# Performance work log

Hardware: AMD Instinct MI355X
Metric: run time of the kernel (lower is better)

Reference implementation:

```python
import jax, jax.numpy as jnp
import numpy as np

H = 1024
E = 8
K = 2
N = 16384
LN_EPS = 1e-5


def _layernorm(h, g, b):
    m = jnp.mean(h, axis=-1, keepdims=True)
    v = jnp.mean(jnp.square(h - m), axis=-1, keepdims=True)
    return (h - m) * jax.lax.rsqrt(v + LN_EPS) * g + b


def setup_inputs() -> dict:
    key = jax.random.key(0)
    ks = jax.random.split(key, 8)
    s = 0.02
    return {
        "x": jax.random.normal(ks[0], (N, H), dtype=jnp.float32),
        "Wg": jax.random.normal(ks[1], (H, E), dtype=jnp.float32) * s,
        "bg": jnp.zeros((E,), dtype=jnp.float32),
        "W1": jax.random.normal(ks[2], (E, H, H), dtype=jnp.float32) * s,
        "b1": jnp.zeros((E, H), dtype=jnp.float32),
        "g1": jnp.ones((E, H), dtype=jnp.float32),
        "be1": jnp.zeros((E, H), dtype=jnp.float32),
        "W2": jax.random.normal(ks[3], (E, H, H), dtype=jnp.float32) * s,
        "b2": jnp.zeros((E, H), dtype=jnp.float32),
        "g2": jnp.ones((E, H), dtype=jnp.float32),
        "be2": jnp.zeros((E, H), dtype=jnp.float32),
    }


def reference(x, Wg, bg, W1, b1, g1, be1, W2, b2, g2, be2):
    # Gating: softmax over experts, top-k, renormalize
    gate_probs = jax.nn.softmax(x @ Wg + bg, axis=1)            # [N, E]
    tk_p, tk_i = jax.lax.top_k(gate_probs, K)                    # [N, K]
    tk_p = tk_p / (jnp.sum(tk_p, axis=1, keepdims=True) + 1e-9)
    # Dense per-expert combine weight (zero where expert not selected)
    w = jnp.sum(tk_p[:, :, None] * jax.nn.one_hot(tk_i, E, dtype=x.dtype), axis=1)  # [N, E]

    # ResidualBlock per expert, computed densely for all tokens (dropout = eval/no-op)
    h = jnp.einsum('nh,eho->eno', x, W1) + b1[:, None, :]        # [E, N, H]
    h = jax.nn.relu(_layernorm(h, g1[:, None, :], be1[:, None, :]))
    h = jnp.einsum('enh,eho->eno', h, W2) + b2[:, None, :]
    h = _layernorm(h, g2[:, None, :], be2[:, None, :])
    y = jax.nn.relu(x[None, :, :] + h)                           # [E, N, H]

    moe_out = jnp.einsum('ne,enh->nh', w, y)                     # [N, H]
    return moe_out, gate_probs
```

## Files before the change

kernel.cpp:

```cpp
#include <hip/hip_runtime.h>
#include <cstdint>
#include <cstddef>

constexpr int H_DIM = 1024;
constexpr int NE    = 8;
constexpr int NT    = 16384;
constexpr int NP    = NT * 2;

constexpr int BM = 128, BN = 128, BK = 32;
constexpr int NKT = H_DIM / BK;
constexpr int MAX_WG = (NP / BM + NE) * (H_DIM / BN);

typedef __attribute__((ext_vector_type(8)))  short          short8;
typedef __attribute__((ext_vector_type(8)))  unsigned short ushort8;
typedef __attribute__((ext_vector_type(4)))  float          f32x4;
typedef __attribute__((ext_vector_type(16))) float          f32x16;

__device__ __forceinline__ unsigned short f2bf(float f) {
  union { float f; uint32_t u; } c; c.f = f;
  uint32_t u = c.u;
  u = (u + 0x7fffu + ((u >> 16) & 1u)) >> 16;
  return (unsigned short)u;
}
__device__ __forceinline__ float bf2f(unsigned short h) {
  union { uint32_t u; float f; } c; c.u = ((uint32_t)h) << 16;
  return c.f;
}

__device__ __forceinline__ void gload16(const unsigned short* g, unsigned short* l) {
  __builtin_amdgcn_global_load_lds((const __attribute__((address_space(1))) void*)g,
                                   (__attribute__((address_space(3))) void*)l, 16, 0, 0);
}

__global__ __launch_bounds__(256) void prep_kernel(
    const float* __restrict__ X, const float* __restrict__ Wg,
    const float* __restrict__ bg, unsigned short* __restrict__ Xb,
    float* __restrict__ gate_out, int* __restrict__ tk_e, float* __restrict__ tk_w,
    const float* __restrict__ W1, const float* __restrict__ W2,
    unsigned short* __restrict__ T1, unsigned short* __restrict__ T2)
{
  __shared__ float tile[64][65];
  int b = blockIdx.x;
  if (b >= 4096) {
    int t = b - 4096;
    int zi = t >> 8;
    const float* W = (zi < 8) ? W1 : W2;
    unsigned short* T = (zi < 8) ? T1 : T2;
    int e  = zi & 7;
    int o0 = ((t >> 4) & 15) * 64;
    int h0 = (t & 15) * 64;
    int c  = threadIdx.x & 63;
    int r0 = (threadIdx.x >> 6) * 16;
    const float* src = W + ((size_t)e * H_DIM + h0) * H_DIM + o0;
#pragma unroll
    for (int i = 0; i < 16; ++i)
      tile[r0 + i][c] = src[(size_t)(r0 + i) * H_DIM + c];
    __syncthreads();
    unsigned short* dst = T + ((size_t)e * H_DIM + o0) * H_DIM + h0;
#pragma unroll
    for (int i = 0; i < 16; ++i)
      dst[(size_t)(r0 + i) * H_DIM + c] = f2bf(tile[c][r0 + i]);
    return;
  }

  int wid = threadIdx.x >> 6, lane = threadIdx.x & 63;
  int n = b * 4 + wid;
  const float* xr = X + (size_t)n * H_DIM;

  const float4* xp = (const float4*)(xr + lane * 16);
  float4 f0 = xp[0], f1 = xp[1], f2 = xp[2], f3 = xp[3];
  float v[16] = {f0.x,f0.y,f0.z,f0.w, f1.x,f1.y,f1.z,f1.w,
                 f2.x,f2.y,f2.z,f2.w, f3.x,f3.y,f3.z,f3.w};

  ushort8 u0, u1;
#pragma unroll
  for (int j = 0; j < 8; ++j) { u0[j] = f2bf(v[j]); u1[j] = f2bf(v[8 + j]); }
  ushort8* xb = (ushort8*)(Xb + (size_t)n * H_DIM + lane * 16);
  xb[0] = u0; xb[1] = u1;

  float acc[8];
#pragma unroll
  for (int e = 0; e < 8; ++e) acc[e] = 0.f;
#pragma unroll
  for (int j = 0; j < 16; ++j) {
    int h = lane * 16 + j;
    const float4* wg = (const float4*)(Wg + (size_t)h * 8);
    float4 a = wg[0], bb = wg[1];
    float xv = v[j];
    acc[0] += xv * a.x;  acc[1] += xv * a.y;  acc[2] += xv * a.z;  acc[3] += xv * a.w;
    acc[4] += xv * bb.x; acc[5] += xv * bb.y; acc[6] += xv * bb.z; acc[7] += xv * bb.w;
  }
#pragma unroll
  for (int m = 1; m < 64; m <<= 1) {
#pragma unroll
    for (int e = 0; e < 8; ++e) acc[e] += __shfl_xor(acc[e], m);
  }
#pragma unroll
  for (int e = 0; e < 8; ++e) acc[e] += bg[e];

  float mx = acc[0];
#pragma unroll
  for (int e = 1; e < 8; ++e) mx = fmaxf(mx, acc[e]);
  float g[8], s = 0.f;
#pragma unroll
  for (int e = 0; e < 8; ++e) { g[e] = __expf(acc[e] - mx); s += g[e]; }
  float inv = 1.f / s;
#pragma unroll
  for (int e = 0; e < 8; ++e) g[e] *= inv;

  int e0 = 0; float b0 = g[0];
#pragma unroll
  for (int e = 1; e < 8; ++e) if (g[e] > b0) { b0 = g[e]; e0 = e; }
  int e1 = -1; float b1v = -1.f;
#pragma unroll
  for (int e = 0; e < 8; ++e) if (e != e0 && g[e] > b1v) { b1v = g[e]; e1 = e; }
  float s2 = b0 + b1v + 1e-9f;

  if (lane == 0) {
    float4* gp = (float4*)(gate_out + (size_t)n * 8);
    gp[0] = make_float4(g[0], g[1], g[2], g[3]);
    gp[1] = make_float4(g[4], g[5], g[6], g[7]);
    tk_e[2 * n] = e0; tk_e[2 * n + 1] = e1;
    tk_w[2 * n] = b0 / s2; tk_w[2 * n + 1] = b1v / s2;
  }
}

__global__ __launch_bounds__(256) void hist_kernel(
    const int* __restrict__ tk_e, int* __restrict__ blockHist)
{
  __shared__ int h[8];
  if (threadIdx.x < 8) h[threadIdx.x] = 0;
  __syncthreads();
  int i0 = blockIdx.x * 512 + threadIdx.x;
  atomicAdd(&h[tk_e[i0]], 1);
  atomicAdd(&h[tk_e[i0 + 256]], 1);
  __syncthreads();
  if (threadIdx.x < 8) blockHist[blockIdx.x * 8 + threadIdx.x] = h[threadIdx.x];
}

__global__ void scan_worklist_kernel(const int* __restrict__ blockHist,
                                     int* __restrict__ blockBase,
                                     int* __restrict__ count, int* __restrict__ offs,
                                     int* __restrict__ wl, int* __restrict__ wlCount)
{
  __shared__ int nmt[8], ebase[8], totalS;
  int e = threadIdx.x;
  if (e < 8) {
    int run = 0;
    for (int b = 0; b < 64; ++b) { blockBase[b * 8 + e] = run; run += blockHist[b * 8 + e]; }
    count[e] = run;
  }
  __syncthreads();
  if (threadIdx.x == 0) {
    int o = 0, wo = 0;
    for (int k = 0; k < 8; ++k) {
      offs[k] = o; o += count[k];
      nmt[k] = (count[k] + BM - 1) / BM;
      ebase[k] = wo; wo += nmt[k] * (H_DIM / BN);
    }
    totalS = wo; wlCount[0] = wo;
  }
  __syncthreads();
  if (e < 8) {
    int o = offs[e];
    for (int b = 0; b < 64; ++b) blockBase[b * 8 + e] += o;
  }
  int total = totalS;
  for (int i = threadIdx.x; i < total; i += blockDim.x) {
    int ee = 0;
    while (ee < 7 && i >= ebase[ee + 1]) ++ee;
    int loc = i - ebase[ee];
    int nt = loc / nmt[ee];
    int mt = loc - nt * nmt[ee];
    wl[i] = (ee << 20) | (nt << 16) | mt;
  }
}

__global__ __launch_bounds__(256) void place_kernel(
    const int* __restrict__ tk_e, const int* __restrict__ blockBase,
    int* __restrict__ pairTok, int* __restrict__ pairExp, int* __restrict__ slots)
{
  __shared__ int cur[8];
  if (threadIdx.x < 8) cur[threadIdx.x] = blockBase[blockIdx.x * 8 + threadIdx.x];
  __syncthreads();
#pragma unroll
  for (int j = 0; j < 2; ++j) {
    int i = blockIdx.x * 512 + j * 256 + threadIdx.x;
    int e = tk_e[i];
    int s = atomicAdd(&cur[e], 1);
    pairTok[s] = i >> 1; pairExp[s] = e; slots[i] = s;
  }
}

template<bool GATHER>
__global__ __launch_bounds__(256, 3) void gemm32_kernel(
    const unsigned short* __restrict__ Ab,
    const unsigned short* __restrict__ Bt,
    const float* __restrict__ bias,
    const int* __restrict__ pairTok,
    const int* __restrict__ count, const int* __restrict__ offs,
    const int* __restrict__ wl, const int* __restrict__ wlCount,
    unsigned short* __restrict__ Out)
{
  __shared__ unsigned short As[3 * 4096];
  __shared__ unsigned short Bs[3 * 4096];

  const int total = wlCount[0];
  const int orig = blockIdx.x;
  if (orig >= total) return;
  const int qq = total >> 3, rr = total & 7;
  const int xcd = orig & 7, sub = orig >> 3;
  const int idx = (xcd < rr ? xcd * (qq + 1) : rr * (qq + 1) + (xcd - rr) * qq) + sub;
  const int ent = wl[idx];
  const int e = ent >> 20, ntb = (ent >> 16) & 15, mtb = ent & 0xffff;
  const int cnt = count[e], base = offs[e];

  const int tid = threadIdx.x;
  const int wid = tid >> 6, l = tid & 63;
  const int wr = wid >> 1, wc = wid & 1;

  const int rsub = (l >> 2);
  const int kswz = ((l & 3) * 8) ^ (((l >> 5) & 1) << 4);

  const unsigned short *apg0, *apg1, *bpg0, *bpg1;
  {
    int r0 = wid * 16 + rsub;
    int r1 = 64 + wid * 16 + rsub;
    int g0 = mtb * BM + r0; if (g0 >= cnt) g0 = cnt - 1;
    int g1 = mtb * BM + r1; if (g1 >= cnt) g1 = cnt - 1;
    size_t a0, a1;
    if (GATHER) { a0 = (size_t)pairTok[base + g0]; a1 = (size_t)pairTok[base + g1]; }
    else        { a0 = (size_t)(base + g0);        a1 = (size_t)(base + g1); }
    apg0 = Ab + a0 * H_DIM + kswz;
    apg1 = Ab + a1 * H_DIM + kswz;
    const unsigned short* bb = Bt + ((size_t)e * H_DIM + ntb * BN) * H_DIM + kswz;
    bpg0 = bb + (size_t)r0 * H_DIM;
    bpg1 = bb + (size_t)r1 * H_DIM;
  }

  const int lrow = (l & 15) * 64 + ((l >> 4) & 1) * 1024;
  const int sw = ((l >> 3) & 1) << 5;
  const int kb0 = (((l >> 5) * 16) + 0)  ^ sw;
  const int kb1 = (((l >> 5) * 16) + 32) ^ sw;

  auto STAGE = [&](int u, int sl) {
    unsigned short* ad = As + sl * 4096 + wid * 512;
    unsigned short* bd = Bs + sl * 4096 + wid * 512;
    gload16(apg0 + (size_t)u * BK, ad);
    gload16(apg1 + (size_t)u * BK, ad + 2048);
    gload16(bpg0 + (size_t)u * BK, bd);
    gload16(bpg1 + (size_t)u * BK, bd + 2048);
  };

  STAGE(0, 0); STAGE(1, 1);
  asm volatile("s_waitcnt vmcnt(4)" ::: "memory");
  __builtin_amdgcn_s_barrier();

  f32x16 acc[2][2] = {};

  int sl = 0, sstage = 2;
  for (int t = 0; t < NKT; ++t) {
    const char* aB = (const char*)As + sl * 8192 + wr * 4096 + lrow;
    const char* bB = (const char*)Bs + sl * 8192 + wc * 4096 + lrow;

    short8 af[2][2], bf[2][2];
#pragma unroll
    for (int j = 0; j < 2; ++j) {
      af[j][0] = *(const short8*)(aB + j * 2048 + kb0);
      af[j][1] = *(const short8*)(aB + j * 2048 + kb1);
      bf[j][0] = *(const short8*)(bB + j * 2048 + kb0);
      bf[j][1] = *(const short8*)(bB + j * 2048 + kb1);
    }

    if (t + 2 < NKT) STAGE(t + 2, sstage);

    __builtin_amdgcn_s_setprio(1);
#pragma unroll
    for (int ks = 0; ks < 2; ++ks)
#pragma unroll
      for (int j = 0; j < 2; ++j)
#pragma unroll
        for (int r = 0; r < 2; ++r)
          acc[j][r] = __builtin_amdgcn_mfma_f32_32x32x16_bf16(af[j][ks], bf[r][ks], acc[j][r], 0, 0, 0);
    __builtin_amdgcn_s_setprio(0);

    if (t + 2 < NKT)       asm volatile("s_waitcnt vmcnt(4)" ::: "memory");
    else if (t + 2 == NKT) asm volatile("s_waitcnt vmcnt(0)" ::: "memory");
    __builtin_amdgcn_s_barrier();

    sl = (sl == 2) ? 0 : sl + 1;
    sstage = (sstage == 2) ? 0 : sstage + 1;
  }

  float bvv[2];
#pragma unroll
  for (int r = 0; r < 2; ++r)
    bvv[r] = bias[e * H_DIM + ntb * BN + wc * 64 + r * 32 + (l & 31)];
#pragma unroll
  for (int j = 0; j < 2; ++j)
#pragma unroll
    for (int r = 0; r < 2; ++r) {
      int gcol = ntb * BN + wc * 64 + r * 32 + (l & 31);
#pragma unroll
      for (int reg = 0; reg < 16; ++reg) {
        int row = mtb * BM + wr * 64 + j * 32 + (reg & 3) + 8 * (reg >> 2) + 4 * (l >> 5);
        if (row < cnt)
          Out[(size_t)(base + row) * H_DIM + gcol] = f2bf(acc[j][r][reg] + bvv[r]);
      }
    }
}

__global__ __launch_bounds__(256) void ln_relu_kernel(
    unsigned short* __restrict__ buf, const float* __restrict__ gamma,
    const float* __restrict__ beta, const int* __restrict__ pairExp)
{
  int wid = threadIdx.x >> 6, lane = threadIdx.x & 63;
  int row = blockIdx.x * 4 + wid;
  int e = pairExp[row];
  unsigned short* r = buf + (size_t)row * H_DIM;
  ushort8 u0 = ((const ushort8*)r)[lane];
  ushort8 u1 = ((const ushort8*)r)[lane + 64];
  float v[16];
#pragma unroll
  for (int j = 0; j < 8; ++j) { v[j] = bf2f(u0[j]); v[8 + j] = bf2f(u1[j]); }
  float s = 0.f, ss = 0.f;
#pragma unroll
  for (int j = 0; j < 16; ++j) { s += v[j]; ss += v[j] * v[j]; }
#pragma unroll
  for (int m = 1; m < 64; m <<= 1) { s += __shfl_xor(s, m); ss += __shfl_xor(ss, m); }
  float mean = s * (1.f / 1024.f);
  float var  = ss * (1.f / 1024.f) - mean * mean;
  float rs   = rsqrtf(var + 1e-5f);

  int h0 = lane * 8, h1 = 512 + lane * 8;
  const float4* gp0 = (const float4*)(gamma + (size_t)e * H_DIM + h0);
  const float4* bp0 = (const float4*)(beta  + (size_t)e * H_DIM + h0);
  const float4* gp1 = (const float4*)(gamma + (size_t)e * H_DIM + h1);
  const float4* bp1 = (const float4*)(beta  + (size_t)e * H_DIM + h1);
  float4 ga = gp0[0], gb = gp0[1], gc = gp1[0], gd = gp1[1];
  float4 ba = bp0[0], bb = bp0[1], bc = bp1[0], bd = bp1[1];
  float gv[16] = {ga.x,ga.y,ga.z,ga.w, gb.x,gb.y,gb.z,gb.w,
                  gc.x,gc.y,gc.z,gc.w, gd.x,gd.y,gd.z,gd.w};
  float bv[16] = {ba.x,ba.y,ba.z,ba.w, bb.x,bb.y,bb.z,bb.w,
                  bc.x,bc.y,bc.z,bc.w, bd.x,bd.y,bd.z,bd.w};
#pragma unroll
  for (int j = 0; j < 8; ++j) {
    float t0 = fmaxf((v[j]     - mean) * rs * gv[j]     + bv[j],     0.f);
    float t1 = fmaxf((v[8 + j] - mean) * rs * gv[8 + j] + bv[8 + j], 0.f);
    u0[j] = f2bf(t0); u1[j] = f2bf(t1);
  }
  ((ushort8*)r)[lane] = u0; ((ushort8*)r)[lane + 64] = u1;
}

__global__ __launch_bounds__(256) void combine_kernel(
    const unsigned short* __restrict__ buf2, const float* __restrict__ X,
    const float* __restrict__ g2, const float* __restrict__ be2,
    const int* __restrict__ slots, const int* __restrict__ tk_e,
    const float* __restrict__ tk_w, float* __restrict__ out)
{
  int wid = threadIdx.x >> 6, lane = threadIdx.x & 63;
  int n = blockIdx.x * 4 + wid;
  int h0 = lane * 8, h1 = 512 + lane * 8;

  const float4* xp0 = (const float4*)(X + (size_t)n * H_DIM + h0);
  const float4* xp1 = (const float4*)(X + (size_t)n * H_DIM + h1);
  float4 xa = xp0[0], xb = xp0[1], xc = xp1[0], xd = xp1[1];
  float xv[16] = {xa.x,xa.y,xa.z,xa.w, xb.x,xb.y,xb.z,xb.w,
                  xc.x,xc.y,xc.z,xc.w, xd.x,xd.y,xd.z,xd.w};
  float o[16];
#pragma unroll
  for (int j = 0; j < 16; ++j) o[j] = 0.f;

#pragma unroll
  for (int k = 0; k < 2; ++k) {
    int slot = slots[2 * n + k];
    int e = tk_e[2 * n + k];
    float w = tk_w[2 * n + k];
    const unsigned short* r = buf2 + (size_t)slot * H_DIM;
    ushort8 u0 = ((const ushort8*)r)[lane];
    ushort8 u1 = ((const ushort8*)r)[lane + 64];
    float v[16];
#pragma unroll
    for (int j = 0; j < 8; ++j) { v[j] = bf2f(u0[j]); v[8 + j] = bf2f(u1[j]); }
    float s = 0.f, ss = 0.f;
#pragma unroll
    for (int j = 0; j < 16; ++j) { s += v[j]; ss += v[j] * v[j]; }
#pragma unroll
    for (int m = 1; m < 64; m <<= 1) { s += __shfl_xor(s, m); ss += __shfl_xor(ss, m); }
    float mean = s * (1.f / 1024.f);
    float var  = ss * (1.f / 1024.f) - mean * mean;
    float rs   = rsqrtf(var + 1e-5f);

    const float4* gp0 = (const float4*)(g2  + (size_t)e * H_DIM + h0);
    const float4* bp0 = (const float4*)(be2 + (size_t)e * H_DIM + h0);
    const float4* gp1 = (const float4*)(g2  + (size_t)e * H_DIM + h1);
    const float4* bp1 = (const float4*)(be2 + (size_t)e * H_DIM + h1);
    float4 ga = gp0[0], gb = gp0[1], gc = gp1[0], gd = gp1[1];
    float4 ba = bp0[0], bb = bp0[1], bc = bp1[0], bd = bp1[1];
    float gv[16] = {ga.x,ga.y,ga.z,ga.w, gb.x,gb.y,gb.z,gb.w,
                    gc.x,gc.y,gc.z,gc.w, gd.x,gd.y,gd.z,gd.w};
    float bvv[16] = {ba.x,ba.y,ba.z,ba.w, bb.x,bb.y,bb.z,bb.w,
                     bc.x,bc.y,bc.z,bc.w, bd.x,bd.y,bd.z,bd.w};
#pragma unroll
    for (int j = 0; j < 16; ++j) {
      float u = (v[j] - mean) * rs * gv[j] + bvv[j];
      float y = fmaxf(xv[j] + u, 0.f);
      o[j] += w * y;
    }
  }

  float4* op0 = (float4*)(out + (size_t)n * H_DIM + h0);
  float4* op1 = (float4*)(out + (size_t)n * H_DIM + h1);
  op0[0] = make_float4(o[0], o[1], o[2], o[3]);
  op0[1] = make_float4(o[4], o[5], o[6], o[7]);
  op1[0] = make_float4(o[8], o[9], o[10], o[11]);
  op1[1] = make_float4(o[12], o[13], o[14], o[15]);
}

extern "C" void kernel_launch(void* const* d_in, const int* in_sizes, int n_in,
                              void* d_out, int out_size, void* d_ws, size_t ws_size,
                              hipStream_t stream)
{
  const float* x   = (const float*)d_in[0];
  const float* Wg  = (const float*)d_in[1];
  const float* bg  = (const float*)d_in[2];
  const float* W1  = (const float*)d_in[3];
  const float* b1  = (const float*)d_in[4];
  const float* g1  = (const float*)d_in[5];
  const float* be1 = (const float*)d_in[6];
  const float* W2  = (const float*)d_in[7];
  const float* b2  = (const float*)d_in[8];
  const float* g2  = (const float*)d_in[9];
  const float* be2 = (const float*)d_in[10];
  float* out = (float*)d_out;
  float* gate_out = out + (size_t)NT * H_DIM;

  char* ws = (char*)d_ws;
  size_t off = 0;
  auto alloc = [&](size_t bytes) { char* p = ws + off; off += (bytes + 255) & ~(size_t)255; return p; };
  unsigned short* w1bt = (unsigned short*)alloc((size_t)NE * H_DIM * H_DIM * 2);
  unsigned short* w2bt = (unsigned short*)alloc((size_t)NE * H_DIM * H_DIM * 2);
  unsigned short* buf1 = (unsigned short*)alloc((size_t)NP * H_DIM * 2);
  unsigned short* buf2 = (unsigned short*)alloc((size_t)NP * H_DIM * 2);
  int*   tk_e      = (int*)alloc((size_t)NP * 4);
  float* tk_w      = (float*)alloc((size_t)NP * 4);
  int*   pairTok   = (int*)alloc((size_t)NP * 4);
  int*   pairExp   = (int*)alloc((size_t)NP * 4);
  int*   slots     = (int*)alloc((size_t)NP * 4);
  int*   blockHist = (int*)alloc(64 * 8 * 4);
  int*   blockBase = (int*)alloc(64 * 8 * 4);
  int*   count     = (int*)alloc(8 * 4);
  int*   offs      = (int*)alloc(8 * 4);
  int*   wl        = (int*)alloc(MAX_WG * 4);
  int*   wlCount   = (int*)alloc(4);
  (void)in_sizes; (void)n_in; (void)out_size; (void)ws_size;

  unsigned short* Xb = buf2;

  prep_kernel<<<dim3(8192), 256, 0, stream>>>(
      x, Wg, bg, Xb, gate_out, tk_e, tk_w, W1, W2, w1bt, w2bt);
  hist_kernel<<<dim3(64), 256, 0, stream>>>(tk_e, blockHist);
  scan_worklist_kernel<<<dim3(1), 256, 0, stream>>>(blockHist, blockBase, count, offs, wl, wlCount);
  place_kernel<<<dim3(64), 256, 0, stream>>>(tk_e, blockBase, pairTok, pairExp, slots);
  gemm32_kernel<true><<<dim3(MAX_WG), 256, 0, stream>>>(
      Xb, w1bt, b1, pairTok, count, offs, wl, wlCount, buf1);
  ln_relu_kernel<<<dim3(NP / 4), 256, 0, stream>>>(buf1, g1, be1, pairExp);
  gemm32_kernel<false><<<dim3(MAX_WG), 256, 0, stream>>>(
      buf1, w2bt, b2, pairTok, count, offs, wl, wlCount, buf2);
  combine_kernel<<<dim3(NT / 4), 256, 0, stream>>>(
      buf2, x, g2, be2, slots, tk_e, tk_w, out);
}
```

Baseline: 392.6 us.

## Make grouped GEMM persistent with atomic tile queue and overlapped epilogue

```diff
diff --git a/kernel.cpp b/kernel.cpp
--- a/kernel.cpp
+++ b/kernel.cpp
@@ -10,11 +10,11 @@
 constexpr int BM = 128, BN = 128, BK = 32;
 constexpr int NKT = H_DIM / BK;
 constexpr int MAX_WG = (NP / BM + NE) * (H_DIM / BN);
+constexpr int GEMM_GRID = 768;
 
 typedef __attribute__((ext_vector_type(8)))  short          short8;
 typedef __attribute__((ext_vector_type(8)))  unsigned short ushort8;
 typedef __attribute__((ext_vector_type(4)))  float          f32x4;
-typedef __attribute__((ext_vector_type(16))) float          f32x16;
 
 __device__ __forceinline__ unsigned short f2bf(float f) {
   union { float f; uint32_t u; } c; c.f = f;
@@ -141,7 +141,8 @@
 __global__ void scan_worklist_kernel(const int* __restrict__ blockHist,
                                      int* __restrict__ blockBase,
                                      int* __restrict__ count, int* __restrict__ offs,
-                                     int* __restrict__ wl, int* __restrict__ wlCount)
+                                     int* __restrict__ wl, int* __restrict__ wlCount,
+                                     int* __restrict__ gemmCtr)
 {
   __shared__ int nmt[8], ebase[8], totalS;
   int e = threadIdx.x;
@@ -159,6 +160,7 @@
       ebase[k] = wo; wo += nmt[k] * (H_DIM / BN);
     }
     totalS = wo; wlCount[0] = wo;
+    gemmCtr[0] = 0; gemmCtr[1] = 0;
   }
   __syncthreads();
   if (e < 8) {
@@ -193,37 +195,36 @@
 }
 
 template<bool GATHER>
-__global__ __launch_bounds__(256, 3) void gemm32_kernel(
+__global__ __launch_bounds__(256, 3) void gemmp_kernel(
     const unsigned short* __restrict__ Ab,
     const unsigned short* __restrict__ Bt,
     const float* __restrict__ bias,
     const int* __restrict__ pairTok,
     const int* __restrict__ count, const int* __restrict__ offs,
     const int* __restrict__ wl, const int* __restrict__ wlCount,
+    int* __restrict__ ctr,
     unsigned short* __restrict__ Out)
 {
   __shared__ unsigned short As[3 * 4096];
   __shared__ unsigned short Bs[3 * 4096];
+  __shared__ int shIdx;
 
   const int total = wlCount[0];
-  const int orig = blockIdx.x;
-  if (orig >= total) return;
-  const int qq = total >> 3, rr = total & 7;
-  const int xcd = orig & 7, sub = orig >> 3;
-  const int idx = (xcd < rr ? xcd * (qq + 1) : rr * (qq + 1) + (xcd - rr) * qq) + sub;
-  const int ent = wl[idx];
-  const int e = ent >> 20, ntb = (ent >> 16) & 15, mtb = ent & 0xffff;
-  const int cnt = count[e], base = offs[e];
-
   const int tid = threadIdx.x;
   const int wid = tid >> 6, l = tid & 63;
   const int wr = wid >> 1, wc = wid & 1;
 
   const int rsub = (l >> 2);
   const int kswz = ((l & 3) * 8) ^ (((l >> 5) & 1) << 4);
-
-  const unsigned short *apg0, *apg1, *bpg0, *bpg1;
-  {
+  const int loff = ((l & 15) * 64 + (l >> 4) * 16) ^ (((l >> 3) & 1) << 5);
+
+  int e = 0, ntb = 0, mtb = 0, cnt = 0, base = 0;
+  const unsigned short *apg0 = nullptr, *apg1 = nullptr, *bpg0 = nullptr, *bpg1 = nullptr;
+
+  auto SETUP = [&](int widx) {
+    int ent = wl[widx];
+    e = ent >> 20; ntb = (ent >> 16) & 15; mtb = ent & 0xffff;
+    cnt = count[e]; base = offs[e];
     int r0 = wid * 16 + rsub;
     int r1 = 64 + wid * 16 + rsub;
     int g0 = mtb * BM + r0; if (g0 >= cnt) g0 = cnt - 1;
@@ -236,78 +237,89 @@
     const unsigned short* bb = Bt + ((size_t)e * H_DIM + ntb * BN) * H_DIM + kswz;
     bpg0 = bb + (size_t)r0 * H_DIM;
     bpg1 = bb + (size_t)r1 * H_DIM;
-  }
-
-  const int lrow = (l & 15) * 64 + ((l >> 4) & 1) * 1024;
-  const int sw = ((l >> 3) & 1) << 5;
-  const int kb0 = (((l >> 5) * 16) + 0)  ^ sw;
-  const int kb1 = (((l >> 5) * 16) + 32) ^ sw;
-
-  auto STAGE = [&](int u, int sl) {
-    unsigned short* ad = As + sl * 4096 + wid * 512;
-    unsigned short* bd = Bs + sl * 4096 + wid * 512;
+  };
+
+  auto STAGE = [&](int u, int slot) {
+    unsigned short* ad = As + slot * 4096 + wid * 512;
+    unsigned short* bd = Bs + slot * 4096 + wid * 512;
     gload16(apg0 + (size_t)u * BK, ad);
     gload16(apg1 + (size_t)u * BK, ad + 2048);
     gload16(bpg0 + (size_t)u * BK, bd);
     gload16(bpg1 + (size_t)u * BK, bd + 2048);
   };
 
+  if (tid == 0) shIdx = atomicAdd(ctr, 1);
+  __syncthreads();
+  int idx = shIdx;
+  if (idx >= total) return;
+
+  SETUP(idx);
   STAGE(0, 0); STAGE(1, 1);
-  asm volatile("s_waitcnt vmcnt(4)" ::: "memory");
-  __builtin_amdgcn_s_barrier();
-
-  f32x16 acc[2][2] = {};
-
-  int sl = 0, sstage = 2;
-  for (int t = 0; t < NKT; ++t) {
-    const char* aB = (const char*)As + sl * 8192 + wr * 4096 + lrow;
-    const char* bB = (const char*)Bs + sl * 8192 + wc * 4096 + lrow;
-
-    short8 af[2][2], bf[2][2];
-#pragma unroll
-    for (int j = 0; j < 2; ++j) {
-      af[j][0] = *(const short8*)(aB + j * 2048 + kb0);
-      af[j][1] = *(const short8*)(aB + j * 2048 + kb1);
-      bf[j][0] = *(const short8*)(bB + j * 2048 + kb0);
-      bf[j][1] = *(const short8*)(bB + j * 2048 + kb1);
+
+  while (true) {
+    asm volatile("s_waitcnt vmcnt(4)" ::: "memory");
+    __builtin_amdgcn_s_barrier();
+
+    f32x4 acc[4][4] = {};
+
+    int sl = 0, sstage = 2;
+    for (int t = 0; t < NKT; ++t) {
+      const char* aB = (const char*)As + sl * 8192 + wr * 4096 + loff;
+      const char* bB = (const char*)Bs + sl * 8192 + wc * 4096 + loff;
+
+      short8 af[4], bfr[4];
+#pragma unroll
+      for (int j = 0; j < 4; ++j) af[j] = *(const short8*)(aB + j * 1024);
+#pragma unroll
+      for (int r = 0; r < 4; ++r) bfr[r] = *(const short8*)(bB + r * 1024);
+
+      if (t + 2 < NKT) STAGE(t + 2, sstage);
+
+      __builtin_amdgcn_s_setprio(1);
+#pragma unroll
+      for (int j = 0; j < 4; ++j)
+#pragma unroll
+        for (int r = 0; r < 4; ++r)
+          acc[j][r] = __builtin_amdgcn_mfma_f32_16x16x32_bf16(af[j], bfr[r], acc[j][r], 0, 0, 0);
+      __builtin_amdgcn_s_setprio(0);
+
+      if (t + 2 < NKT)       asm volatile("s_waitcnt vmcnt(4)" ::: "memory");
+      else if (t + 2 == NKT) asm volatile("s_waitcnt vmcnt(0)" ::: "memory");
+      __builtin_amdgcn_s_barrier();
+
+      sl = (sl == 2) ? 0 : sl + 1;
+      sstage = (sstage == 2) ? 0 : sstage + 1;
     }
 
-    if (t + 2 < NKT) STAGE(t + 2, sstage);
-
-    __builtin_amdgcn_s_setprio(1);
-#pragma unroll
-    for (int ks = 0; ks < 2; ++ks)
-#pragma unroll
-      for (int j = 0; j < 2; ++j)
-#pragma unroll
-        for (int r = 0; r < 2; ++r)
-          acc[j][r] = __builtin_amdgcn_mfma_f32_32x32x16_bf16(af[j][ks], bf[r][ks], acc[j][r], 0, 0, 0);
-    __builtin_amdgcn_s_setprio(0);
-
-    if (t + 2 < NKT)       asm volatile("s_waitcnt vmcnt(4)" ::: "memory");
-    else if (t + 2 == NKT) asm volatile("s_waitcnt vmcnt(0)" ::: "memory");
-    __builtin_amdgcn_s_barrier();
-
-    sl = (sl == 2) ? 0 : sl + 1;
-    sstage = (sstage == 2) ? 0 : sstage + 1;
-  }
-
-  float bvv[2];
-#pragma unroll
-  for (int r = 0; r < 2; ++r)
-    bvv[r] = bias[e * H_DIM + ntb * BN + wc * 64 + r * 32 + (l & 31)];
-#pragma unroll
-  for (int j = 0; j < 2; ++j)
-#pragma unroll
-    for (int r = 0; r < 2; ++r) {
-      int gcol = ntb * BN + wc * 64 + r * 32 + (l & 31);
-#pragma unroll
-      for (int reg = 0; reg < 16; ++reg) {
-        int row = mtb * BM + wr * 64 + j * 32 + (reg & 3) + 8 * (reg >> 2) + 4 * (l >> 5);
-        if (row < cnt)
-          Out[(size_t)(base + row) * H_DIM + gcol] = f2bf(acc[j][r][reg] + bvv[r]);
+    if (tid == 0) shIdx = atomicAdd(ctr, 1);
+    __syncthreads();
+    int nidx = shIdx;
+    bool more = (nidx < total);
+
+    int ce = e, cntb = ntb, cmtb = mtb, ccnt = cnt, cbase = base;
+    if (more) { SETUP(nidx); STAGE(0, 0); STAGE(1, 1); }
+
+    float bvv[4];
+#pragma unroll
+    for (int r = 0; r < 4; ++r)
+      bvv[r] = bias[ce * H_DIM + cntb * BN + wc * 64 + r * 16 + (l & 15)];
+#pragma unroll
+    for (int j = 0; j < 4; ++j) {
+      int grow0 = cmtb * BM + wr * 64 + j * 16 + (l >> 4) * 4;
+#pragma unroll
+      for (int r = 0; r < 4; ++r) {
+        int gcol = cntb * BN + wc * 64 + r * 16 + (l & 15);
+#pragma unroll
+        for (int v = 0; v < 4; ++v) {
+          int row = grow0 + v;
+          if (row < ccnt)
+            Out[(size_t)(cbase + row) * H_DIM + gcol] = f2bf(acc[j][r][v] + bvv[r]);
+        }
       }
     }
+
+    if (!more) return;
+  }
 }
 
 __global__ __launch_bounds__(256) void ln_relu_kernel(
@@ -453,6 +465,7 @@
   int*   offs      = (int*)alloc(8 * 4);
   int*   wl        = (int*)alloc(MAX_WG * 4);
   int*   wlCount   = (int*)alloc(4);
+  int*   gemmCtr   = (int*)alloc(2 * 4);
   (void)in_sizes; (void)n_in; (void)out_size; (void)ws_size;
 
   unsigned short* Xb = buf2;
@@ -460,13 +473,14 @@
   prep_kernel<<<dim3(8192), 256, 0, stream>>>(
       x, Wg, bg, Xb, gate_out, tk_e, tk_w, W1, W2, w1bt, w2bt);
   hist_kernel<<<dim3(64), 256, 0, stream>>>(tk_e, blockHist);
-  scan_worklist_kernel<<<dim3(1), 256, 0, stream>>>(blockHist, blockBase, count, offs, wl, wlCount);
+  scan_worklist_kernel<<<dim3(1), 256, 0, stream>>>(
+      blockHist, blockBase, count, offs, wl, wlCount, gemmCtr);
   place_kernel<<<dim3(64), 256, 0, stream>>>(tk_e, blockBase, pairTok, pairExp, slots);
-  gemm32_kernel<true><<<dim3(MAX_WG), 256, 0, stream>>>(
-      Xb, w1bt, b1, pairTok, count, offs, wl, wlCount, buf1);
+  gemmp_kernel<true><<<dim3(GEMM_GRID), 256, 0, stream>>>(
+      Xb, w1bt, b1, pairTok, count, offs, wl, wlCount, gemmCtr + 0, buf1);
   ln_relu_kernel<<<dim3(NP / 4), 256, 0, stream>>>(buf1, g1, be1, pairExp);
-  gemm32_kernel<false><<<dim3(MAX_WG), 256, 0, stream>>>(
-      buf1, w2bt, b2, pairTok, count, offs, wl, wlCount, buf2);
+  gemmp_kernel<false><<<dim3(GEMM_GRID), 256, 0, stream>>>(
+      buf1, w2bt, b2, pairTok, count, offs, wl, wlCount, gemmCtr + 1, buf2);
   combine_kernel<<<dim3(NT / 4), 256, 0, stream>>>(
       buf2, x, g2, be2, slots, tk_e, tk_w, out);
 }
```

Result: slower. 421.6 us (+7.4%).
